# Kernel tuning notes

Measured on AMD Instinct MI355X. Metric: run time of the kernel, lower is better.

## Reference

```python
import jax, jax.numpy as jnp
import numpy as np

B, N, E = 8, 5000, 40000
F, FE, FILTERS = 64, 16, 96
LN_EPS = 1e-3  # keras LayerNormalization default epsilon


def _layer_norm(x, gamma, beta):
    mu = jnp.mean(x, axis=-1, keepdims=True)
    var = jnp.mean(jnp.square(x - mu), axis=-1, keepdims=True)
    return (x - mu) * jax.lax.rsqrt(var + LN_EPS) * gamma + beta


def setup_inputs() -> dict:
    key = jax.random.key(0)
    ks = jax.random.split(key, 8)
    nodes = jax.random.normal(ks[0], (B, N, F), dtype=jnp.float32)
    edge_features = jax.random.normal(ks[1], (B, E, FE), dtype=jnp.float32)
    edges = jax.random.randint(ks[2], (B, E, 2), 0, N, dtype=jnp.int32)
    d_msg_in = 2 * F + FE   # 144
    d_upd_in = F + FILTERS  # 160
    Wm = jax.random.normal(ks[3], (d_msg_in, FILTERS), dtype=jnp.float32) / np.sqrt(d_msg_in)
    bm = jnp.zeros((FILTERS,), dtype=jnp.float32)
    Wu = jax.random.normal(ks[4], (d_upd_in, FILTERS), dtype=jnp.float32) / np.sqrt(d_upd_in)
    bu = jnp.zeros((FILTERS,), dtype=jnp.float32)
    ln_m_gamma = jnp.ones((FILTERS,), dtype=jnp.float32)
    ln_m_beta = jnp.zeros((FILTERS,), dtype=jnp.float32)
    ln_u_gamma = jnp.ones((FILTERS,), dtype=jnp.float32)
    ln_u_beta = jnp.zeros((FILTERS,), dtype=jnp.float32)
    return {"nodes": nodes, "edge_features": edge_features, "edges": edges,
            "Wm": Wm, "bm": bm, "ln_m_gamma": ln_m_gamma, "ln_m_beta": ln_m_beta,
            "Wu": Wu, "bu": bu, "ln_u_gamma": ln_u_gamma, "ln_u_beta": ln_u_beta}


def reference(nodes, edge_features, edges, Wm, bm, ln_m_gamma, ln_m_beta,
              Wu, bu, ln_u_gamma, ln_u_beta):
    b, n, f = nodes.shape
    e = edges.shape[1]
    # gather endpoint features: (B,E,2,F) -> (B,E,2F)   [tf.gather batch_dims=1 + reshape]
    gathered = jax.vmap(lambda nd, ed: nd[ed])(nodes, edges)
    messages_in = gathered.reshape(b, e, 2 * f)
    msg_in = jnp.concatenate([messages_in, edge_features], axis=-1)
    # message layer: Dense -> relu -> LayerNorm
    messages = jax.nn.relu(jnp.einsum('bec,cd->bed', msg_in, Wm) + bm)
    messages = _layer_norm(messages, ln_m_gamma, ln_m_beta)
    # aggregate: per-batch unsorted_segment_sum over destination node edges[...,1]
    aggregated = jax.vmap(
        lambda m, dst: jax.ops.segment_sum(m, dst, num_segments=n)
    )(messages, edges[..., 1])
    # update layer on [nodes, aggregated]: Dense -> relu -> LayerNorm
    upd_in = jnp.concatenate([nodes, aggregated], axis=-1)
    updated = jax.nn.relu(jnp.einsum('bnc,cd->bnd', upd_in, Wu) + bu)
    updated_nodes = _layer_norm(updated, ln_u_gamma, ln_u_beta)
    return updated_nodes, messages
```

## Files before the change

kernel.cpp:

```cpp
#include <hip/hip_runtime.h>
#include <hip/hip_bf16.h>

typedef short s16x8 __attribute__((ext_vector_type(8)));
typedef float f32x4 __attribute__((ext_vector_type(4)));

namespace {
constexpr int kB   = 8;
constexpr int kN   = 5000;
constexpr int kE   = 40000;
constexpr int kF   = 64;
constexpr int kFE  = 16;
constexpr int kFil = 96;
constexpr float kEps = 1e-3f;
constexpr int kBN = kB * kN;
constexpr int kBE = kB * kE;
constexpr int kKp = 160;
constexpr int kLd = 168;
constexpr int kBM = 128;
}

__device__ inline unsigned short f2bf(float x) {
    unsigned u = __float_as_uint(x);
    u += 0x7FFFu + ((u >> 16) & 1u);
    return (unsigned short)(u >> 16);
}

__device__ inline s16x8 pack8(const float4& a, const float4& b) {
    union { s16x8 s; __hip_bfloat162 h[4]; } r;
    r.h[0] = __float22bfloat162_rn(make_float2(a.x, a.y));
    r.h[1] = __float22bfloat162_rn(make_float2(a.z, a.w));
    r.h[2] = __float22bfloat162_rn(make_float2(b.x, b.y));
    r.h[3] = __float22bfloat162_rn(make_float2(b.z, b.w));
    return r.s;
}

__device__ inline s16x8 loadA8(const float* __restrict__ p) {
    const float4* q = reinterpret_cast<const float4*>(p);
    return pack8(q[0], q[1]);
}

__global__ void prep_wT(const float* __restrict__ Wm, const float* __restrict__ Wu,
                        short* __restrict__ wmT, short* __restrict__ wuT) {
    const int t = blockIdx.x * 256 + threadIdx.x;
    if (t >= 96 * kKp) return;
    const int n = t / kKp, k = t % kKp;
    wmT[t] = (k < 144) ? (short)f2bf(Wm[(size_t)k * 96 + n]) : (short)0;
    wuT[t] = (short)f2bf(Wu[(size_t)k * 96 + n]);
}

__device__ inline void gemm_ln_store(const s16x8 a[5], const short* sB,
                                     const float* __restrict__ bias,
                                     const float* __restrict__ gamma_,
                                     const float* __restrict__ beta_,
                                     float* __restrict__ out,
                                     int rowBase, int rowMax) {
    const int tid  = threadIdx.x;
    const int w    = tid >> 6;
    const int lane = tid & 63;
    const int cl   = lane & 15;
    const int quad = lane >> 4;

    f32x4 acc[6] = {};
#pragma unroll
    for (int ks = 0; ks < 5; ++ks) {
#pragma unroll
        for (int t = 0; t < 6; ++t) {
            s16x8 b = *reinterpret_cast<const s16x8*>(
                sB + (16 * t + cl) * kLd + ks * 32 + quad * 8);
            acc[t] = __builtin_amdgcn_mfma_f32_16x16x32_bf16(a[ks], b, acc[t], 0, 0, 0);
        }
    }

    float bmv[6], gv[6], bv[6];
#pragma unroll
    for (int t = 0; t < 6; ++t) {
        const int c = 16 * t + cl;
        bmv[t] = bias[c]; gv[t] = gamma_[c]; bv[t] = beta_[c];
    }
#pragma unroll
    for (int j = 0; j < 4; ++j) {
        float v0[6];
        float s = 0.f;
#pragma unroll
        for (int t = 0; t < 6; ++t) {
            v0[t] = fmaxf(acc[t][j] + bmv[t], 0.f);
            s += v0[t];
        }
        s += __shfl_xor(s, 1); s += __shfl_xor(s, 2);
        s += __shfl_xor(s, 4); s += __shfl_xor(s, 8);
        const float mu = s * (1.f / 96.f);
        float q = 0.f;
#pragma unroll
        for (int t = 0; t < 6; ++t) {
            const float d = v0[t] - mu;
            q = fmaf(d, d, q);
        }
        q += __shfl_xor(q, 1); q += __shfl_xor(q, 2);
        q += __shfl_xor(q, 4); q += __shfl_xor(q, 8);
        const float inv = rsqrtf(q * (1.f / 96.f) + kEps);
        const int row = rowBase + 16 * w + 4 * quad + j;
        if (row < rowMax) {
            float* orow = out + (size_t)row * kFil;
#pragma unroll
            for (int t = 0; t < 6; ++t)
                orow[16 * t + cl] = (v0[t] - mu) * inv * gv[t] + bv[t];
        }
    }
}

__global__ __launch_bounds__(512, 4) void msg_gemm(
    const float* __restrict__ nodes, const float* __restrict__ efeat,
    const int* __restrict__ edges, const short* __restrict__ wmT,
    const float* __restrict__ bm, const float* __restrict__ g,
    const float* __restrict__ be, float* __restrict__ out_msg) {
    __shared__ short sB[96 * kLd];
    const int tid  = threadIdx.x;
    const int w    = tid >> 6;
    const int lane = tid & 63;
    const int cl   = lane & 15;
    const int quad = lane >> 4;

    const int row = blockIdx.x * kBM + 16 * w + cl;
    const int b   = row / kE;
    const int2 e2 = reinterpret_cast<const int2*>(edges)[row];
    const float* srcp = nodes + ((size_t)b * kN + e2.x) * kF + 8 * quad;
    const float* dstp = nodes + ((size_t)b * kN + e2.y) * kF + 8 * quad;

    s16x8 a[5];
    a[0] = loadA8(srcp);
    a[1] = loadA8(srcp + 32);
    a[2] = loadA8(dstp);
    a[3] = loadA8(dstp + 32);
    if (quad < 2) {
        a[4] = loadA8(efeat + (size_t)row * kFE + 8 * quad);
    } else {
        s16x8 z = {};
        a[4] = z;
    }

    for (int i = tid; i < 96 * kKp / 8; i += 512) {
        const int n = i / 20, c = i % 20;
        *reinterpret_cast<s16x8*>(sB + n * kLd + 8 * c) =
            *reinterpret_cast<const s16x8*>(wmT + n * kKp + 8 * c);
    }
    __syncthreads();
    gemm_ln_store(a, sB, bm, g, be, out_msg, blockIdx.x * kBM, kBE);
}

__global__ __launch_bounds__(256) void scatter_pk(
    const float* __restrict__ out_msg, const int* __restrict__ edges,
    short* __restrict__ agg) {
    const int idx  = blockIdx.x * 256 + threadIdx.x;
    const int edge = idx / 48;
    const int pair = idx - edge * 48;
    const int b    = edge / kE;
    const int dn   = edges[(size_t)edge * 2 + 1];
    const float2 v = reinterpret_cast<const float2*>(
        out_msg + (size_t)edge * kFil)[pair];
    __hip_bfloat162 hv = __float22bfloat162_rn(make_float2(v.x, v.y));
    unsigned dw;
    __builtin_memcpy(&dw, &hv, 4);
    short* addr = agg + ((size_t)b * kN + dn) * kFil + 2 * pair;
    asm volatile("global_atomic_pk_add_bf16 %0, %1, off"
                 :: "v"((unsigned long long)addr), "v"(dw) : "memory");
}

__global__ __launch_bounds__(512, 4) void upd_mfma(
    const float* __restrict__ nodes, const short* __restrict__ agg,
    const short* __restrict__ wuT, const float* __restrict__ bu,
    const float* __restrict__ g, const float* __restrict__ be,
    float* __restrict__ out_upd) {
    __shared__ short sB[96 * kLd];
    const int tid  = threadIdx.x;
    const int w    = tid >> 6;
    const int lane = tid & 63;
    const int cl   = lane & 15;
    const int quad = lane >> 4;

    const int node0 = blockIdx.x * kBM + 16 * w + cl;
    const int node  = (node0 < kBN) ? node0 : (kBN - 1);
    const float* np = nodes + (size_t)node * kF + 8 * quad;
    const short* ap = agg + (size_t)node * kFil;

    s16x8 a[5];
    a[0] = loadA8(np);
    a[1] = loadA8(np + 32);
    a[2] = *reinterpret_cast<const s16x8*>(ap + 8 * quad);
    a[3] = *reinterpret_cast<const s16x8*>(ap + 32 + 8 * quad);
    a[4] = *reinterpret_cast<const s16x8*>(ap + 64 + 8 * quad);

    for (int i = tid; i < 96 * kKp / 8; i += 512) {
        const int n = i / 20, c = i % 20;
        *reinterpret_cast<s16x8*>(sB + n * kLd + 8 * c) =
            *reinterpret_cast<const s16x8*>(wuT + n * kKp + 8 * c);
    }
    __syncthreads();
    gemm_ln_store(a, sB, bu, g, be, out_upd, blockIdx.x * kBM, kBN);
}

extern "C" void kernel_launch(void* const* d_in, const int* in_sizes, int n_in,
                              void* d_out, int out_size, void* d_ws, size_t ws_size,
                              hipStream_t stream) {
    const float* nodes  = (const float*)d_in[0];
    const float* efeat  = (const float*)d_in[1];
    const int*   edges  = (const int*)d_in[2];
    const float* Wm     = (const float*)d_in[3];
    const float* bm     = (const float*)d_in[4];
    const float* ln_m_g = (const float*)d_in[5];
    const float* ln_m_b = (const float*)d_in[6];
    const float* Wu     = (const float*)d_in[7];
    const float* bu     = (const float*)d_in[8];
    const float* ln_u_g = (const float*)d_in[9];
    const float* ln_u_b = (const float*)d_in[10];

    float* out_upd = (float*)d_out;
    float* out_msg = (float*)d_out + (size_t)kBN * kFil;

    short* wmT = (short*)d_ws;
    short* wuT = wmT + 96 * kKp;
    short* agg = wuT + 96 * kKp;

    hipMemsetAsync(agg, 0, (size_t)kBN * kFil * sizeof(short), stream);
    prep_wT<<<(96 * kKp + 255) / 256, 256, 0, stream>>>(Wm, Wu, wmT, wuT);

    msg_gemm<<<kBE / kBM, 512, 0, stream>>>(
        nodes, efeat, edges, wmT, bm, ln_m_g, ln_m_b, out_msg);
    scatter_pk<<<kBE * 48 / 256, 256, 0, stream>>>(out_msg, edges, agg);
    upd_mfma<<<(kBN + kBM - 1) / kBM, 512, 0, stream>>>(
        nodes, agg, wuT, bu, ln_u_g, ln_u_b, out_upd);
}
```

Before: 276.0 us.

## Double rows per message block, fuse memset into weight prep, pair-vectorize output stores

The message GEMM now handles 256 edges per block, with two accumulator sets per wave sharing each B fragment read from LDS. This halves the per-block weight staging and the number of blocks. The hipMemsetAsync of the aggregation buffer is folded into the weight-transpose kernel, removing one launch. LayerNorm outputs are written as float2 by pairing adjacent lanes with a shuffle. Costs are higher register pressure (the occupancy hint of 4 is dropped) and fewer blocks in the grid.

```diff
diff --git a/kernel.cpp b/kernel.cpp
--- a/kernel.cpp
+++ b/kernel.cpp
@@ -17,6 +17,7 @@
 constexpr int kKp = 160;
 constexpr int kLd = 168;
 constexpr int kBM = 128;
+constexpr int kBM2 = 256;
 }
 
 __device__ inline unsigned short f2bf(float x) {
@@ -39,44 +40,27 @@
     return pack8(q[0], q[1]);
 }
 
-__global__ void prep_wT(const float* __restrict__ Wm, const float* __restrict__ Wu,
-                        short* __restrict__ wmT, short* __restrict__ wuT) {
+__global__ __launch_bounds__(256) void prep_zero(
+    const float* __restrict__ Wm, const float* __restrict__ Wu,
+    short* __restrict__ wmT, short* __restrict__ wuT,
+    s16x8* __restrict__ aggz) {
     const int t = blockIdx.x * 256 + threadIdx.x;
-    if (t >= 96 * kKp) return;
-    const int n = t / kKp, k = t % kKp;
-    wmT[t] = (k < 144) ? (short)f2bf(Wm[(size_t)k * 96 + n]) : (short)0;
-    wuT[t] = (short)f2bf(Wu[(size_t)k * 96 + n]);
-}
-
-__device__ inline void gemm_ln_store(const s16x8 a[5], const short* sB,
-                                     const float* __restrict__ bias,
-                                     const float* __restrict__ gamma_,
-                                     const float* __restrict__ beta_,
-                                     float* __restrict__ out,
-                                     int rowBase, int rowMax) {
-    const int tid  = threadIdx.x;
-    const int w    = tid >> 6;
-    const int lane = tid & 63;
-    const int cl   = lane & 15;
-    const int quad = lane >> 4;
-
-    f32x4 acc[6] = {};
-#pragma unroll
-    for (int ks = 0; ks < 5; ++ks) {
-#pragma unroll
-        for (int t = 0; t < 6; ++t) {
-            s16x8 b = *reinterpret_cast<const s16x8*>(
-                sB + (16 * t + cl) * kLd + ks * 32 + quad * 8);
-            acc[t] = __builtin_amdgcn_mfma_f32_16x16x32_bf16(a[ks], b, acc[t], 0, 0, 0);
-        }
-    }
-
-    float bmv[6], gv[6], bv[6];
-#pragma unroll
-    for (int t = 0; t < 6; ++t) {
-        const int c = 16 * t + cl;
-        bmv[t] = bias[c]; gv[t] = gamma_[c]; bv[t] = beta_[c];
-    }
+    if (t < 96 * kKp) {
+        const int n = t / kKp, k = t % kKp;
+        wmT[t] = (k < 144) ? (short)f2bf(Wm[(size_t)k * 96 + n]) : (short)0;
+        wuT[t] = (short)f2bf(Wu[(size_t)k * 96 + n]);
+    }
+    if (t < kBN * kFil / 8) {
+        s16x8 z = {};
+        aggz[t] = z;
+    }
+}
+
+__device__ inline void ln_epilogue(const f32x4 acc[6],
+                                   const float bmv[6], const float gv[6],
+                                   const float bv[6],
+                                   float* __restrict__ out,
+                                   int row0, int cl, int rowMax) {
 #pragma unroll
     for (int j = 0; j < 4; ++j) {
         float v0[6];
@@ -98,17 +82,26 @@
         q += __shfl_xor(q, 1); q += __shfl_xor(q, 2);
         q += __shfl_xor(q, 4); q += __shfl_xor(q, 8);
         const float inv = rsqrtf(q * (1.f / 96.f) + kEps);
-        const int row = rowBase + 16 * w + 4 * quad + j;
+        const int row = row0 + j;
         if (row < rowMax) {
             float* orow = out + (size_t)row * kFil;
+            float ov[6];
 #pragma unroll
             for (int t = 0; t < 6; ++t)
-                orow[16 * t + cl] = (v0[t] - mu) * inv * gv[t] + bv[t];
-        }
-    }
-}
-
-__global__ __launch_bounds__(512, 4) void msg_gemm(
+                ov[t] = (v0[t] - mu) * inv * gv[t] + bv[t];
+#pragma unroll
+            for (int t = 0; t < 6; ++t) {
+                const float other = __shfl_xor(ov[t], 1);
+                if ((cl & 1) == 0) {
+                    float2 st; st.x = ov[t]; st.y = other;
+                    *reinterpret_cast<float2*>(orow + 16 * t + cl) = st;
+                }
+            }
+        }
+    }
+}
+
+__global__ __launch_bounds__(512) void msg_gemm(
     const float* __restrict__ nodes, const float* __restrict__ efeat,
     const int* __restrict__ edges, const short* __restrict__ wmT,
     const float* __restrict__ bm, const float* __restrict__ g,
@@ -120,22 +113,28 @@
     const int cl   = lane & 15;
     const int quad = lane >> 4;
 
-    const int row = blockIdx.x * kBM + 16 * w + cl;
-    const int b   = row / kE;
-    const int2 e2 = reinterpret_cast<const int2*>(edges)[row];
-    const float* srcp = nodes + ((size_t)b * kN + e2.x) * kF + 8 * quad;
-    const float* dstp = nodes + ((size_t)b * kN + e2.y) * kF + 8 * quad;
-
-    s16x8 a[5];
-    a[0] = loadA8(srcp);
-    a[1] = loadA8(srcp + 32);
-    a[2] = loadA8(dstp);
-    a[3] = loadA8(dstp + 32);
+    const int rA0 = blockIdx.x * kBM2 + 16 * w + cl;
+    const int rA1 = rA0 + 128;
+    const int b0  = rA0 / kE;
+    const int b1  = rA1 / kE;
+    const int2 e0 = reinterpret_cast<const int2*>(edges)[rA0];
+    const int2 e1 = reinterpret_cast<const int2*>(edges)[rA1];
+    const float* s0p = nodes + ((size_t)b0 * kN + e0.x) * kF + 8 * quad;
+    const float* d0p = nodes + ((size_t)b0 * kN + e0.y) * kF + 8 * quad;
+    const float* s1p = nodes + ((size_t)b1 * kN + e1.x) * kF + 8 * quad;
+    const float* d1p = nodes + ((size_t)b1 * kN + e1.y) * kF + 8 * quad;
+
+    s16x8 a0[5], a1[5];
+    a0[0] = loadA8(s0p);       a1[0] = loadA8(s1p);
+    a0[1] = loadA8(s0p + 32);  a1[1] = loadA8(s1p + 32);
+    a0[2] = loadA8(d0p);       a1[2] = loadA8(d1p);
+    a0[3] = loadA8(d0p + 32);  a1[3] = loadA8(d1p + 32);
     if (quad < 2) {
-        a[4] = loadA8(efeat + (size_t)row * kFE + 8 * quad);
+        a0[4] = loadA8(efeat + (size_t)rA0 * kFE + 8 * quad);
+        a1[4] = loadA8(efeat + (size_t)rA1 * kFE + 8 * quad);
     } else {
         s16x8 z = {};
-        a[4] = z;
+        a0[4] = z; a1[4] = z;
     }
 
     for (int i = tid; i < 96 * kKp / 8; i += 512) {
@@ -144,7 +143,28 @@
             *reinterpret_cast<const s16x8*>(wmT + n * kKp + 8 * c);
     }
     __syncthreads();
-    gemm_ln_store(a, sB, bm, g, be, out_msg, blockIdx.x * kBM, kBE);
+
+    f32x4 acc0[6] = {}, acc1[6] = {};
+#pragma unroll
+    for (int ks = 0; ks < 5; ++ks) {
+#pragma unroll
+        for (int t = 0; t < 6; ++t) {
+            s16x8 bfr = *reinterpret_cast<const s16x8*>(
+                sB + (16 * t + cl) * kLd + ks * 32 + quad * 8);
+            acc0[t] = __builtin_amdgcn_mfma_f32_16x16x32_bf16(a0[ks], bfr, acc0[t], 0, 0, 0);
+            acc1[t] = __builtin_amdgcn_mfma_f32_16x16x32_bf16(a1[ks], bfr, acc1[t], 0, 0, 0);
+        }
+    }
+
+    float bmv[6], gv[6], bv[6];
+#pragma unroll
+    for (int t = 0; t < 6; ++t) {
+        const int c = 16 * t + cl;
+        bmv[t] = bm[c]; gv[t] = g[c]; bv[t] = be[c];
+    }
+    const int row0 = blockIdx.x * kBM2 + 16 * w + 4 * quad;
+    ln_epilogue(acc0, bmv, gv, bv, out_msg, row0,       cl, kBE);
+    ln_epilogue(acc1, bmv, gv, bv, out_msg, row0 + 128, cl, kBE);
 }
 
 __global__ __launch_bounds__(256) void scatter_pk(
@@ -195,7 +215,26 @@
             *reinterpret_cast<const s16x8*>(wuT + n * kKp + 8 * c);
     }
     __syncthreads();
-    gemm_ln_store(a, sB, bu, g, be, out_upd, blockIdx.x * kBM, kBN);
+
+    f32x4 acc[6] = {};
+#pragma unroll
+    for (int ks = 0; ks < 5; ++ks) {
+#pragma unroll
+        for (int t = 0; t < 6; ++t) {
+            s16x8 bfr = *reinterpret_cast<const s16x8*>(
+                sB + (16 * t + cl) * kLd + ks * 32 + quad * 8);
+            acc[t] = __builtin_amdgcn_mfma_f32_16x16x32_bf16(a[ks], bfr, acc[t], 0, 0, 0);
+        }
+    }
+
+    float bmv[6], gv[6], bv[6];
+#pragma unroll
+    for (int t = 0; t < 6; ++t) {
+        const int c = 16 * t + cl;
+        bmv[t] = bu[c]; gv[t] = g[c]; bv[t] = be[c];
+    }
+    ln_epilogue(acc, bmv, gv, bv, out_upd,
+                blockIdx.x * kBM + 16 * w + 4 * quad, cl, kBN);
 }
 
 extern "C" void kernel_launch(void* const* d_in, const int* in_sizes, int n_in,
@@ -220,10 +259,10 @@
     short* wuT = wmT + 96 * kKp;
     short* agg = wuT + 96 * kKp;
 
-    hipMemsetAsync(agg, 0, (size_t)kBN * kFil * sizeof(short), stream);
-    prep_wT<<<(96 * kKp + 255) / 256, 256, 0, stream>>>(Wm, Wu, wmT, wuT);
-
-    msg_gemm<<<kBE / kBM, 512, 0, stream>>>(
+    prep_zero<<<(kBN * kFil / 8 + 255) / 256, 256, 0, stream>>>(
+        Wm, Wu, wmT, wuT, (s16x8*)agg);
+
+    msg_gemm<<<kBE / kBM2, 512, 0, stream>>>(
         nodes, efeat, edges, wmT, bm, ln_m_g, ln_m_b, out_msg);
     scatter_pk<<<kBE * 48 / 256, 256, 0, stream>>>(out_msg, edges, agg);
     upd_mfma<<<(kBN + kBM - 1) / kBM, 512, 0, stream>>>(
```

Measured after the change: 272.0 us. About the same (-1.4%).
